# Optimization experiments

Hardware: AMD Instinct MI355X
Metric: run time of the kernel (lower is better)

## Reference

```python
import jax, jax.numpy as jnp
import numpy as np

B, S, D, H, FF = 4, 2048, 512, 8, 2048
DK = D // H
EPS = 1e-6


def _ln(x, g, b):
    mu = jnp.mean(x, axis=-1, keepdims=True)
    var = jnp.mean(jnp.square(x - mu), axis=-1, keepdims=True)
    return (x - mu) * jax.lax.rsqrt(var + EPS) * g + b


def setup_inputs() -> dict:
    key = jax.random.key(0)
    ks = jax.random.split(key, 12)
    s_qkv = 1.0 / np.sqrt(2.0) * np.sqrt(6.0 / (D + D))  # xavier_uniform gain=1/sqrt(2)
    s_ff1 = np.sqrt(1.0 / D)
    s_ff2 = np.sqrt(1.0 / FF)
    u = lambda k, shape, s: jax.random.uniform(k, shape, jnp.float32, -s, s)
    return {
        "x": jax.random.normal(ks[0], (B, S, D), jnp.float32),
        "Wq": u(ks[1], (D, D), s_qkv),
        "Wk": u(ks[2], (D, D), s_qkv),
        "Wv": u(ks[3], (D, D), s_qkv),
        "Wo": u(ks[4], (D, D), s_qkv),
        "bo": jnp.zeros((D,), jnp.float32),
        "g1": jnp.ones((D,), jnp.float32),
        "b1": jnp.zeros((D,), jnp.float32),
        "g2": jnp.ones((D,), jnp.float32),
        "b2": jnp.zeros((D,), jnp.float32),
        "W1": u(ks[5], (D, FF), s_ff1),
        "bf1": u(ks[6], (FF,), s_ff1),
        "W2": u(ks[7], (FF, D), s_ff2),
        "bf2": u(ks[8], (D,), s_ff2),
    }


def reference(x, Wq, Wk, Wv, Wo, bo, g1, b1, g2, b2, W1, bf1, W2, bf2):
    # --- pre-norm attention ---
    xn = _ln(x, g1, b1)                                   # [B,S,D]
    q = (xn @ Wq).reshape(B, S, H, DK).transpose(0, 2, 1, 3)  # [B,H,S,DK]
    k = (xn @ Wk).reshape(B, S, H, DK).transpose(0, 2, 1, 3)
    v = (xn @ Wv).reshape(B, S, H, DK).transpose(0, 2, 1, 3)
    scores = jnp.einsum("bhqd,bhkd->bhqk", q, k) / jnp.sqrt(jnp.float32(DK))
    attn = jax.nn.softmax(scores, axis=-1)                # [B,H,S,S] materialized
    ctx = jnp.einsum("bhqk,bhkd->bhqd", attn, v)          # [B,H,S,DK]
    ctx = ctx.transpose(0, 2, 1, 3).reshape(B, S, D)
    x = x + ctx @ Wo + bo
    # --- pre-norm FFN ---
    xn = _ln(x, g2, b2)
    h = jax.nn.gelu(xn @ W1 + bf1, approximate=False)
    x = x + h @ W2 + bf2
    return x
```

## Files before the change

kernel.cpp:

```cpp
#include <hip/hip_runtime.h>
#include <hip/hip_bf16.h>
#include <math.h>

typedef unsigned short u16;
typedef __attribute__((ext_vector_type(8))) unsigned short u16x8;
typedef __attribute__((ext_vector_type(8))) short s16x8;
typedef __attribute__((ext_vector_type(4))) float f32x4;
typedef __attribute__((ext_vector_type(16))) float f32x16;
typedef __attribute__((ext_vector_type(4))) unsigned int u32x4;

#define BB 4
#define SS 2048
#define DD 512
#define HH 8
#define DKK 64
#define FFF 2048

#define QSCALE 0.18033688011112042f

#define GLP(p) ((const __attribute__((address_space(1))) void*)(p))
#define LDP(p) ((__attribute__((address_space(3))) void*)(p))

__device__ __forceinline__ float bf2f(u16 u){
  union { unsigned int i; float f; } x; x.i = ((unsigned int)u)<<16; return x.f;
}
__device__ __forceinline__ u16 f2bf(float f){
  union { float fl; unsigned int i; } x; x.fl = f;
  unsigned int r = x.i + 0x7fffu + ((x.i>>16)&1u);
  return (u16)(r>>16);
}
__device__ __forceinline__ unsigned cvt_pk_bf16(float a, float b){
  unsigned d;
  asm volatile("v_cvt_pk_bf16_f32 %0, %1, %2" : "=v"(d) : "v"(a), "v"(b));
  return d;
}
__device__ __forceinline__ void pl32swap(unsigned &a, unsigned &b){
  asm volatile("v_permlane32_swap_b32 %0, %1" : "+v"(a), "+v"(b));
}

__global__ __launch_bounds__(256) void ln_k(const float* __restrict__ x, const float* __restrict__ g,
                     const float* __restrict__ b, u16* __restrict__ o){
  int row = blockIdx.x*4 + (threadIdx.x>>6);
  int lane = threadIdx.x & 63;
  const float* xr = x + (size_t)row*DD + lane*8;
  float4 v0 = *(const float4*)xr;
  float4 v1 = *(const float4*)(xr+4);
  float f[8] = {v0.x,v0.y,v0.z,v0.w,v1.x,v1.y,v1.z,v1.w};
  float s=0.f, s2=0.f;
#pragma unroll
  for (int i=0;i<8;i++){ s+=f[i]; s2+=f[i]*f[i]; }
#pragma unroll
  for (int off=1; off<64; off<<=1){ s += __shfl_xor(s, off); s2 += __shfl_xor(s2, off); }
  float mu = s * (1.f/DD);
  float var = s2 * (1.f/DD) - mu*mu;
  float rs = rsqrtf(var + 1e-6f);
  float4 g0 = *(const float4*)(g + lane*8);
  float4 g1 = *(const float4*)(g + lane*8 + 4);
  float4 b0 = *(const float4*)(b + lane*8);
  float4 b1 = *(const float4*)(b + lane*8 + 4);
  float gg[8] = {g0.x,g0.y,g0.z,g0.w,g1.x,g1.y,g1.z,g1.w};
  float bb[8] = {b0.x,b0.y,b0.z,b0.w,b1.x,b1.y,b1.z,b1.w};
  u16x8 ov;
#pragma unroll
  for (int i=0;i<8;i++) ov[i] = f2bf((f[i]-mu)*rs*gg[i] + bb[i]);
  *(u16x8*)(o + (size_t)row*DD + lane*8) = ov;
}

__global__ __launch_bounds__(256) void wprep_k(
    const float* __restrict__ Wq, const float* __restrict__ Wk,
    const float* __restrict__ Wv, const float* __restrict__ Wo,
    const float* __restrict__ W1, const float* __restrict__ W2,
    u16* __restrict__ wtq, u16* __restrict__ wtk, u16* __restrict__ wtv,
    u16* __restrict__ wto, u16* __restrict__ wt1, u16* __restrict__ wt2){
  __shared__ u16 tile[64][72];
  int id = blockIdx.x;
  const float* src; u16* dst; int R, C, bx, by;
  if (id < 256){
    int m = id >> 6, s = id & 63;
    src = (m==0)?Wq:(m==1)?Wk:(m==2)?Wv:Wo;
    dst = (m==0)?wtq:(m==1)?wtk:(m==2)?wtv:wto;
    R = 512; C = 512; bx = s&7; by = s>>3;
  } else if (id < 512){
    int s = id - 256; src = W1; dst = wt1; R = 512; C = 2048; bx = s&31; by = s>>5;
  } else {
    int s = id - 512; src = W2; dst = wt2; R = 2048; C = 512; bx = s&7; by = s>>3;
  }
  int r0 = by*64, c0 = bx*64;
  int t = threadIdx.x;
#pragma unroll
  for (int i=0;i<2;i++){
    int u = t + 256*i;
    int r = u>>3, cb = (u&7)*8;
    const float* sp = src + (size_t)(r0+r)*C + c0 + cb;
    float4 v0 = *(const float4*)sp;
    float4 v1 = *(const float4*)(sp+4);
    float f[8] = {v0.x,v0.y,v0.z,v0.w,v1.x,v1.y,v1.z,v1.w};
#pragma unroll
    for (int j=0;j<8;j++) tile[r][cb+j] = f2bf(f[j]);
  }
  __syncthreads();
#pragma unroll
  for (int i=0;i<2;i++){
    int u = t + 256*i;
    int c = u>>3, rb = (u&7)*8;
    u16x8 ov;
#pragma unroll
    for (int j=0;j<8;j++) ov[j] = tile[rb+j][c];
    *(u16x8*)(dst + (size_t)(c0+c)*R + r0 + rb) = ov;
  }
}

__global__ __launch_bounds__(256) void trv_k(const u16* __restrict__ V, u16* __restrict__ Vt){
  __shared__ u16 tile[64][72];
  int bh = blockIdx.y; int b = bh>>3, h = bh&7;
  int s0 = blockIdx.x*64;
  int t = threadIdx.x;
#pragma unroll
  for (int i=0;i<2;i++){
    int u = t + 256*i;
    int r = u>>3, cb = (u&7)*8;
    u16x8 v = *(const u16x8*)(V + ((size_t)(b*SS) + s0 + r)*DD + h*DKK + cb);
#pragma unroll
    for (int j=0;j<8;j++) tile[r][cb+j] = v[j];
  }
  __syncthreads();
#pragma unroll
  for (int i=0;i<2;i++){
    int u = t + 256*i;
    int c = u>>3, rb = (u&7)*8;
    u16x8 ov;
#pragma unroll
    for (int j=0;j<8;j++) ov[j] = tile[rb+j][c];
    *(u16x8*)(Vt + ((size_t)(bh*DKK) + c)*SS + s0 + rb) = ov;
  }
}

__device__ __forceinline__ void xcd_swz(unsigned& bx, unsigned& by, unsigned& bz){
  unsigned nx = gridDim.x, ny = gridDim.y;
  unsigned nwg = nx*ny*gridDim.z;
  unsigned f = blockIdx.x + nx*(blockIdx.y + ny*blockIdx.z);
  unsigned fs = (f & 7)*(nwg >> 3) + (f >> 3);
  bx = fs % nx; unsigned rem = fs / nx;
  by = rem % ny; bz = rem / ny;
}

template<int EPI, int BM>
__global__ __launch_bounds__(256) void gemm_bt(const u16* __restrict__ A, const u16* __restrict__ Bt,
    void* __restrict__ Cv, const float* __restrict__ bias, const float* __restrict__ res,
    int M, int N, int K, long zB, long zC){
  constexpr int NFR = (BM==128) ? 4 : 2;
  unsigned bxs, bys, bzs;
  xcd_swz(bxs, bys, bzs);
  Bt += (size_t)bzs * zB;
  __shared__ u16 la[2][BM*64];
  __shared__ u16 lb[2][128*64];
  int t = threadIdx.x, lane = t&63, w = t>>6;
  int wr = (BM==128) ? (w>>1) : 0;
  int wc = (BM==128) ? (w&1)  : w;
  int m0 = bys*BM, n0 = bxs*128;
  int r = lane&15, g = lane>>4;
  int cbx = ((lane&7) ^ (lane>>3))*16;
  int lrow = lane>>3;
  f32x4 acc[4][NFR];
#pragma unroll
  for (int m=0;m<4;m++)
#pragma unroll
    for (int n=0;n<NFR;n++) acc[m][n] = (f32x4)0.f;

#define GSTAGE(buf, k0) do { \
    _Pragma("unroll") \
    for (int i_=0;i_<4;i_++){ \
      int br_ = 8*w + 32*i_; \
      int row_ = br_ + lrow; \
      if (BM==128 || i_<2) \
        __builtin_amdgcn_global_load_lds( \
          GLP((const char*)(A + (size_t)(m0+row_)*K + (k0)) + cbx), \
          LDP((char*)la[buf] + br_*128), 16, 0, 0); \
      __builtin_amdgcn_global_load_lds( \
        GLP((const char*)(Bt + (size_t)(n0+row_)*K + (k0)) + cbx), \
        LDP((char*)lb[buf] + br_*128), 16, 0, 0); \
    } } while(0)

  GSTAGE(0, 0);
  __syncthreads();
  int nk = K >> 6;
  for (int ki=0; ki<nk; ki++){
    int cur = ki & 1;
    if (ki+1 < nk) GSTAGE(cur^1, (ki+1)*64);
    const u16* lac = la[cur];
    const u16* lbc = lb[cur];
    s16x8 bfr[NFR][2];
#pragma unroll
    for (int n=0;n<NFR;n++)
#pragma unroll
      for (int kk=0;kk<2;kk++){
        int row = wc*(16*NFR) + n*16 + r;
        int cb = kk*64 + g*16;
        bfr[n][kk] = *(const s16x8*)((const char*)lbc + row*128 + (cb ^ ((row&7)<<4)));
      }
#pragma unroll
    for (int m=0;m<4;m++){
      int row = wr*64 + m*16 + r;
      s16x8 a0 = *(const s16x8*)((const char*)lac + row*128 + ((g*16)      ^ ((row&7)<<4)));
      s16x8 a1 = *(const s16x8*)((const char*)lac + row*128 + ((64 + g*16) ^ ((row&7)<<4)));
#pragma unroll
      for (int n=0;n<NFR;n++){
        acc[m][n] = __builtin_amdgcn_mfma_f32_16x16x32_bf16(a0, bfr[n][0], acc[m][n], 0,0,0);
        acc[m][n] = __builtin_amdgcn_mfma_f32_16x16x32_bf16(a1, bfr[n][1], acc[m][n], 0,0,0);
      }
    }
    __syncthreads();
  }
#undef GSTAGE
  float scl = (EPI==0 && bzs==0) ? QSCALE : 1.f;
#pragma unroll
  for (int m=0;m<4;m++)
#pragma unroll
    for (int n=0;n<NFR;n++){
      int col = n0 + wc*(16*NFR) + n*16 + r;
#pragma unroll
      for (int reg=0; reg<4; reg++){
        int row = m0 + wr*64 + m*16 + g*4 + reg;
        float v = acc[m][n][reg];
        if (EPI==1){
          v += bias[col] + res[(size_t)row*N + col];
          ((float*)Cv)[(size_t)row*N + col] = v;
        } else if (EPI==2){
          v += bias[col];
          float y = v*(2.30211416f + 0.10294904f*v*v);
          float sg = 1.f/(1.f + __builtin_amdgcn_exp2f(-y));
          ((u16*)Cv)[(size_t)row*N + col] = f2bf(v*sg);
        } else {
          ((u16*)Cv + (size_t)bzs*zC)[(size_t)row*N + col] = f2bf(v*scl);
        }
      }
    }
}

__global__ __launch_bounds__(256,4) void attn_k(const u16* __restrict__ Q, const u16* __restrict__ Kb,
    const u16* __restrict__ Vt, u16* __restrict__ po, float* __restrict__ pl){
  unsigned bxs, bys, bzs;
  xcd_swz(bxs, bys, bzs);
  int q0 = bxs*128; int h = bys; int b = bzs>>1; int z2 = bzs&1;
  int kbase = z2*(SS/2);
  int t = threadIdx.x, lane = t&63, w = t>>6;
  int l31 = lane&31, lh = lane>>5;
  __shared__ u16 kt[2][64*64];
  __shared__ u16 vt[2][64*64];
  const u16* qbase = Q + ((size_t)(b*SS) + q0 + w*32 + l31)*DD + h*DKK + lh*8;
  s16x8 qf[4];
#pragma unroll
  for (int dblk=0;dblk<4;dblk++) qf[dblk] = *(const s16x8*)(qbase + 16*dblk);
  float l_ = 0.f;
  f32x16 cacc[2];
  cacc[0] = (f32x16)0.f; cacc[1] = (f32x16)0.f;
  int cbx = ((lane&7) ^ (lane>>3) ^ w)*16;
  int lrow = lane>>3;
  int rsw = (l31&7) ^ ((l31>>3)&3);

#define ASTAGE(buf, kk0) do { \
    _Pragma("unroll") \
    for (int i_=0;i_<2;i_++){ \
      int br_ = 8*(w + 4*i_); \
      int row_ = br_ + lrow; \
      __builtin_amdgcn_global_load_lds( \
        GLP((const char*)(Kb + ((size_t)(b*SS) + (kk0) + row_)*DD + h*DKK) + cbx), \
        LDP((char*)kt[buf] + br_*128), 16, 0, 0); \
      __builtin_amdgcn_global_load_lds( \
        GLP((const char*)(Vt + ((size_t)(b*HH+h)*DKK + row_)*SS + (kk0)) + cbx), \
        LDP((char*)vt[buf] + br_*128), 16, 0, 0); \
    } } while(0)

  auto ldk = [&](const u16* base, int blk32, int cb16)->s16x8 {
    int row = blk32*32 + l31;
    int slot = cb16 ^ rsw;
    return *(const s16x8*)((const char*)base + row*128 + slot*16);
  };

  auto tile_compute = [&](const u16* ktc, const u16* vtc){
    f32x16 sc[2];
    sc[0] = (f32x16)0.f; sc[1] = (f32x16)0.f;
    __builtin_amdgcn_s_setprio(1);
#pragma unroll
    for (int kkb=0;kkb<2;kkb++){
#pragma unroll
      for (int dblk=0;dblk<4;dblk++){
        s16x8 kf = ldk(ktc, kkb, 2*dblk + lh);
        sc[kkb] = __builtin_amdgcn_mfma_f32_32x32x16_bf16(kf, qf[dblk], sc[kkb], 0,0,0);
      }
    }
    __builtin_amdgcn_s_setprio(0);
    float ps = 0.f;
#pragma unroll
    for (int kkb=0;kkb<2;kkb++)
#pragma unroll
      for (int i=0;i<16;i++){
        float p = __builtin_amdgcn_exp2f(sc[kkb][i]);
        sc[kkb][i] = p;
        ps += p;
      }
    ps += __shfl_xor(ps, 32);
    l_ += ps;
    unsigned c0[8], c1[8];
#pragma unroll
    for (int i=0;i<8;i++){
      c0[i] = cvt_pk_bf16(sc[0][2*i], sc[0][2*i+1]);
      c1[i] = cvt_pk_bf16(sc[1][2*i], sc[1][2*i+1]);
    }
    s16x8 pa[4];
#pragma unroll
    for (int t_=0;t_<4;t_++){
      unsigned* cc = (t_>>1) ? c1 : c0;
      int s = (t_&1)*4;
      unsigned w0 = cc[s+0], w2 = cc[s+2];
      unsigned w1 = cc[s+1], w3 = cc[s+3];
      pl32swap(w0, w2);
      pl32swap(w1, w3);
      u32x4 fw; fw[0]=w0; fw[1]=w1; fw[2]=w2; fw[3]=w3;
      pa[t_] = __builtin_bit_cast(s16x8, fw);
    }
    __builtin_amdgcn_s_setprio(1);
#pragma unroll
    for (int db=0;db<2;db++){
#pragma unroll
      for (int t_=0;t_<4;t_++){
        s16x8 vf = ldk(vtc, db, 2*t_ + lh);
        cacc[db] = __builtin_amdgcn_mfma_f32_32x32x16_bf16(pa[t_], vf, cacc[db], 0,0,0);
      }
    }
    __builtin_amdgcn_s_setprio(0);
  };

  ASTAGE(0, kbase);
  __syncthreads();
  for (int ti=0; ti<16; ti++){
    int cur = ti & 1;
    if (ti+1 < 16) ASTAGE(cur^1, kbase + (ti+1)*64);
    tile_compute(kt[cur], vt[cur]);
    __syncthreads();
  }
#undef ASTAGE
  {
    size_t pb = (size_t)((z2*BB + b)*SS) + q0 + w*32;
    size_t co = (size_t)h*DKK + l31;
#pragma unroll
    for (int db=0;db<2;db++)
#pragma unroll
      for (int reg=0;reg<16;reg++){
        int qrow = (reg&3) + 8*(reg>>2) + 4*lh;
        po[(pb + qrow)*DD + co + db*32] = f2bf(cacc[db][reg]);
      }
  }
  if (lane < 32){
    size_t lbase = ((size_t)((z2*BB + b)*HH) + h)*SS + q0 + w*32;
    pl[lbase + lane] = l_;
  }
}

__global__ __launch_bounds__(256) void red_k(const u16* __restrict__ po, const float* __restrict__ pl,
                                             u16* __restrict__ ctx){
  int row = blockIdx.x*4 + (threadIdx.x>>6);
  int lane = threadIdx.x & 63;
  int b = row >> 11, s = row & (SS-1);
  int h = lane >> 3;
  u16x8 p0 = *(const u16x8*)(po + ((size_t)((0*BB + b)*SS) + s)*DD + lane*8);
  u16x8 p1 = *(const u16x8*)(po + ((size_t)((1*BB + b)*SS) + s)*DD + lane*8);
  float l0 = pl[((size_t)((0*BB + b)*HH) + h)*SS + s];
  float l1 = pl[((size_t)((1*BB + b)*HH) + h)*SS + s];
  float inv = 1.f/(l0 + l1);
  u16x8 ov;
#pragma unroll
  for (int j=0;j<8;j++) ov[j] = f2bf((bf2f(p0[j]) + bf2f(p1[j]))*inv);
  *(u16x8*)(ctx + (size_t)row*DD + lane*8) = ov;
}

extern "C" void kernel_launch(void* const* d_in, const int* in_sizes, int n_in,
                              void* d_out, int out_size, void* d_ws, size_t ws_size,
                              hipStream_t stream){
  const float* x   = (const float*)d_in[0];
  const float* Wq  = (const float*)d_in[1];
  const float* Wk  = (const float*)d_in[2];
  const float* Wv  = (const float*)d_in[3];
  const float* Wo  = (const float*)d_in[4];
  const float* bo  = (const float*)d_in[5];
  const float* g1  = (const float*)d_in[6];
  const float* b1  = (const float*)d_in[7];
  const float* g2  = (const float*)d_in[8];
  const float* b2  = (const float*)d_in[9];
  const float* W1  = (const float*)d_in[10];
  const float* bf1 = (const float*)d_in[11];
  const float* W2  = (const float*)d_in[12];
  const float* bf2 = (const float*)d_in[13];
  float* out = (float*)d_out;

  char* p = (char*)d_ws;
  u16* wtq = (u16*)p;                p += (size_t)512*512*2;
  u16* wtk = (u16*)p;                p += (size_t)512*512*2;
  u16* wtv = (u16*)p;                p += (size_t)512*512*2;
  u16* wto = (u16*)p;                p += (size_t)512*512*2;
  u16* wt1 = (u16*)p;                p += (size_t)2048*512*2;
  u16* wt2 = (u16*)p;                p += (size_t)512*2048*2;
  u16* xn1 = (u16*)p;                p += (size_t)8192*512*2;
  u16* Qb  = (u16*)p;                p += (size_t)8192*512*2;
  u16* Kb  = (u16*)p;                p += (size_t)8192*512*2;
  u16* Vb  = (u16*)p;                p += (size_t)8192*512*2;
  u16* Vtb = (u16*)p;                p += (size_t)8192*512*2;
  float* x1 = (float*)p;             p += (size_t)8192*512*4;
  float* pl = (float*)p;             p += (size_t)2*BB*HH*SS*4;
  u16* hb  = Qb;
  u16* po  = (u16*)x1;

  dim3 blk(256);
  wprep_k<<<dim3(768), blk, 0, stream>>>(Wq, Wk, Wv, Wo, W1, W2,
                                         wtq, wtk, wtv, wto, wt1, wt2);
  ln_k<<<dim3(2048), blk, 0, stream>>>(x, g1, b1, xn1);
  gemm_bt<0,128><<<dim3(4,64,3), blk, 0, stream>>>(xn1, wtq, Qb, nullptr, nullptr,
                                                   8192,512,512, (long)512*512, (long)8192*512);
  trv_k<<<dim3(32,32), blk, 0, stream>>>(Vb, Vtb);
  attn_k<<<dim3(16,8,8), blk, 0, stream>>>(Qb, Kb, Vtb, po, pl);
  red_k<<<dim3(2048), blk, 0, stream>>>(po, pl, xn1);
  gemm_bt<1,64><<<dim3(4,128,1), blk, 0, stream>>>(xn1, wto, x1, bo, x, 8192,512,512, 0,0);
  ln_k<<<dim3(2048), blk, 0, stream>>>(x1, g2, b2, xn1);
  gemm_bt<2,128><<<dim3(16,64,1), blk, 0, stream>>>(xn1, wt1, hb, bf1, nullptr, 8192,2048,512, 0,0);
  gemm_bt<1,64><<<dim3(4,128,1), blk, 0, stream>>>(hb, wt2, out, bf2, x1, 8192,512,2048, 0,0);
}
```

Baseline: 171.4 us.

## Drop split-K attention and reduction kernel, normalize output inside attention

```diff
diff --git a/kernel.cpp b/kernel.cpp
--- a/kernel.cpp
+++ b/kernel.cpp
@@ -237,16 +237,15 @@
     }
 }
 
-__global__ __launch_bounds__(256,4) void attn_k(const u16* __restrict__ Q, const u16* __restrict__ Kb,
-    const u16* __restrict__ Vt, u16* __restrict__ po, float* __restrict__ pl){
+__global__ __launch_bounds__(256,2) void attn_k(const u16* __restrict__ Q, const u16* __restrict__ Kb,
+    const u16* __restrict__ Vt, u16* __restrict__ ctx){
   unsigned bxs, bys, bzs;
   xcd_swz(bxs, bys, bzs);
-  int q0 = bxs*128; int h = bys; int b = bzs>>1; int z2 = bzs&1;
-  int kbase = z2*(SS/2);
+  int q0 = bxs*128; int h = bys; int b = bzs;
   int t = threadIdx.x, lane = t&63, w = t>>6;
   int l31 = lane&31, lh = lane>>5;
-  __shared__ u16 kt[2][64*64];
-  __shared__ u16 vt[2][64*64];
+  __shared__ u16 kt[2][2][64*64];
+  __shared__ u16 vt[2][2][64*64];
   const u16* qbase = Q + ((size_t)(b*SS) + q0 + w*32 + l31)*DD + h*DKK + lh*8;
   s16x8 qf[4];
 #pragma unroll
@@ -258,17 +257,17 @@
   int lrow = lane>>3;
   int rsw = (l31&7) ^ ((l31>>3)&3);
 
-#define ASTAGE(buf, kk0) do { \
+#define ASTAGE(buf, slot, kk0) do { \
     _Pragma("unroll") \
     for (int i_=0;i_<2;i_++){ \
       int br_ = 8*(w + 4*i_); \
       int row_ = br_ + lrow; \
       __builtin_amdgcn_global_load_lds( \
         GLP((const char*)(Kb + ((size_t)(b*SS) + (kk0) + row_)*DD + h*DKK) + cbx), \
-        LDP((char*)kt[buf] + br_*128), 16, 0, 0); \
+        LDP((char*)kt[buf][slot] + br_*128), 16, 0, 0); \
       __builtin_amdgcn_global_load_lds( \
         GLP((const char*)(Vt + ((size_t)(b*HH+h)*DKK + row_)*SS + (kk0)) + cbx), \
-        LDP((char*)vt[buf] + br_*128), 16, 0, 0); \
+        LDP((char*)vt[buf][slot] + br_*128), 16, 0, 0); \
     } } while(0)
 
   auto ldk = [&](const u16* base, int blk32, int cb16)->s16x8 {
@@ -331,47 +330,32 @@
     __builtin_amdgcn_s_setprio(0);
   };
 
-  ASTAGE(0, kbase);
+  ASTAGE(0, 0, 0);
+  ASTAGE(0, 1, 64);
   __syncthreads();
-  for (int ti=0; ti<16; ti++){
-    int cur = ti & 1;
-    if (ti+1 < 16) ASTAGE(cur^1, kbase + (ti+1)*64);
-    tile_compute(kt[cur], vt[cur]);
+  int cur = 0;
+  for (int ks=0; ks<SS; ks+=128){
+    if (ks+128 < SS){
+      ASTAGE(cur^1, 0, ks+128);
+      ASTAGE(cur^1, 1, ks+192);
+    }
+    tile_compute(kt[cur][0], vt[cur][0]);
+    tile_compute(kt[cur][1], vt[cur][1]);
     __syncthreads();
+    cur ^= 1;
   }
 #undef ASTAGE
   {
-    size_t pb = (size_t)((z2*BB + b)*SS) + q0 + w*32;
+    size_t pb = (size_t)(b*SS) + q0 + w*32;
     size_t co = (size_t)h*DKK + l31;
 #pragma unroll
-    for (int db=0;db<2;db++)
-#pragma unroll
-      for (int reg=0;reg<16;reg++){
-        int qrow = (reg&3) + 8*(reg>>2) + 4*lh;
-        po[(pb + qrow)*DD + co + db*32] = f2bf(cacc[db][reg]);
-      }
-  }
-  if (lane < 32){
-    size_t lbase = ((size_t)((z2*BB + b)*HH) + h)*SS + q0 + w*32;
-    pl[lbase + lane] = l_;
-  }
-}
-
-__global__ __launch_bounds__(256) void red_k(const u16* __restrict__ po, const float* __restrict__ pl,
-                                             u16* __restrict__ ctx){
-  int row = blockIdx.x*4 + (threadIdx.x>>6);
-  int lane = threadIdx.x & 63;
-  int b = row >> 11, s = row & (SS-1);
-  int h = lane >> 3;
-  u16x8 p0 = *(const u16x8*)(po + ((size_t)((0*BB + b)*SS) + s)*DD + lane*8);
-  u16x8 p1 = *(const u16x8*)(po + ((size_t)((1*BB + b)*SS) + s)*DD + lane*8);
-  float l0 = pl[((size_t)((0*BB + b)*HH) + h)*SS + s];
-  float l1 = pl[((size_t)((1*BB + b)*HH) + h)*SS + s];
-  float inv = 1.f/(l0 + l1);
-  u16x8 ov;
-#pragma unroll
-  for (int j=0;j<8;j++) ov[j] = f2bf((bf2f(p0[j]) + bf2f(p1[j]))*inv);
-  *(u16x8*)(ctx + (size_t)row*DD + lane*8) = ov;
+    for (int reg=0;reg<16;reg++){
+      int qrow = (reg&3) + 8*(reg>>2) + 4*lh;
+      float linv = 1.f/__shfl(l_, qrow);
+      ctx[(pb + qrow)*DD + co]      = f2bf(cacc[0][reg]*linv);
+      ctx[(pb + qrow)*DD + co + 32] = f2bf(cacc[1][reg]*linv);
+    }
+  }
 }
 
 extern "C" void kernel_launch(void* const* d_in, const int* in_sizes, int n_in,
@@ -406,9 +390,7 @@
   u16* Vb  = (u16*)p;                p += (size_t)8192*512*2;
   u16* Vtb = (u16*)p;                p += (size_t)8192*512*2;
   float* x1 = (float*)p;             p += (size_t)8192*512*4;
-  float* pl = (float*)p;             p += (size_t)2*BB*HH*SS*4;
   u16* hb  = Qb;
-  u16* po  = (u16*)x1;
 
   dim3 blk(256);
   wprep_k<<<dim3(768), blk, 0, stream>>>(Wq, Wk, Wv, Wo, W1, W2,
@@ -417,8 +399,7 @@
   gemm_bt<0,128><<<dim3(4,64,3), blk, 0, stream>>>(xn1, wtq, Qb, nullptr, nullptr,
                                                    8192,512,512, (long)512*512, (long)8192*512);
   trv_k<<<dim3(32,32), blk, 0, stream>>>(Vb, Vtb);
-  attn_k<<<dim3(16,8,8), blk, 0, stream>>>(Qb, Kb, Vtb, po, pl);
-  red_k<<<dim3(2048), blk, 0, stream>>>(po, pl, xn1);
+  attn_k<<<dim3(16,8,4), blk, 0, stream>>>(Qb, Kb, Vtb, xn1);
   gemm_bt<1,64><<<dim3(4,128,1), blk, 0, stream>>>(xn1, wto, x1, bo, x, 8192,512,512, 0,0);
   ln_k<<<dim3(2048), blk, 0, stream>>>(x1, g2, b2, xn1);
   gemm_bt<2,128><<<dim3(16,64,1), blk, 0, stream>>>(xn1, wt1, hb, bf1, nullptr, 8192,2048,512, 0,0);
```

Result: faster. 162.7 us (-5.1%).
